# Optimization experiments

Measured on AMD Instinct MI355X. Metric: run time of the kernel, lower is better.

## Reference

```python
import jax, jax.numpy as jnp
import numpy as np

# ---- static lookup-point config (matches cfg.radius/stride/level) ----
RADIUS = [4, 4, 4, 4]
STRIDE = [1, 1, 1, 1]
LEVEL = [0, 1, 2, 3]

def _build_pts():
    pts = {}
    for r, s, l in zip(RADIUS, STRIDE, LEVEL):
        pts.setdefault(l, set())
        for x in range(-r, r + 1):
            for y in range(-r, r + 1):
                pts[l].add((x * s, y * s))
    # sorted() reproduces torch's `v.sort()` on (x, y) tuples
    return {l: np.array(sorted(v), dtype=np.float32) for l, v in sorted(pts.items())}

PTS = _build_pts()                       # {lvl: (n_lvl, 2) offsets in level pixels}
N_LEVELS = max(LEVEL) + 1                # 4
CORR_DIM = 2 * sum(len(v) for v in PTS.values())   # 648
C_HALF = CORR_DIM // 2                   # 324 = per-direction channels
B, C, H, W = 1, 256, 80, 80


def _bilinear_sample(corr, x, y):
    """corr: (B, P, h, w); x, y: (P, n) pixel coords (align_corners=False convention,
    already converted to pixel space). Zero padding outside. Returns (B, P, n)."""
    Bn, P, h, w = corr.shape
    cf = corr.reshape(Bn, P, h * w)
    x0 = jnp.floor(x)
    y0 = jnp.floor(y)
    wx1 = x - x0
    wy1 = y - y0
    x0i = x0.astype(jnp.int32)
    y0i = y0.astype(jnp.int32)
    out = jnp.zeros((Bn, P, x.shape[-1]), corr.dtype)
    for dx, wxx in ((0, 1.0 - wx1), (1, wx1)):
        for dy, wyy in ((0, 1.0 - wy1), (1, wy1)):
            xi = x0i + dx
            yi = y0i + dy
            valid = (xi >= 0) & (xi < w) & (yi >= 0) & (yi < h)
            idx = jnp.clip(yi, 0, h - 1) * w + jnp.clip(xi, 0, w - 1)   # (P, n)
            v = jnp.take_along_axis(cf, jnp.broadcast_to(idx[None], (Bn,) + idx.shape), axis=2)
            out = out + v * (wxx * wyy * valid)[None]
    return out


def _lookup_pyramid(pyr):
    """pyr[lvl]: (B, P, H>>lvl, W>>lvl). Returns (B, P, C_HALF)."""
    outs = []
    for lvl, pts in PTS.items():
        s = 1 << lvl
        n = pts.shape[0]
        dxy = jnp.asarray(pts)
        # grid_sample align_corners=False: level-pixel coord of full-res pixel j is
        # (2j+1)/(2s) - 0.5; neighbor offsets are exactly `pts` in level pixels.
        bx = (2.0 * jnp.arange(W) + 1.0) / (2.0 * s) - 0.5   # (W,)
        by = (2.0 * jnp.arange(H) + 1.0) / (2.0 * s) - 0.5   # (H,)
        x = jnp.broadcast_to(bx[None, :, None] + dxy[None, None, :, 0], (H, W, n)).reshape(H * W, n)
        y = jnp.broadcast_to(by[:, None, None] + dxy[None, None, :, 1], (H, W, n)).reshape(H * W, n)
        outs.append(_bilinear_sample(pyr[lvl], x, y))
    return jnp.concatenate(outs, axis=-1)


def _pyramid(corr):
    """corr: (B, P, H, W) -> list of avg-pooled levels (2x2, stride 2)."""
    p = [corr]
    for _ in range(N_LEVELS - 1):
        b, pp, h, w = corr.shape
        corr = corr.reshape(b, pp, h // 2, 2, w // 2, 2).mean(axis=(3, 5))
        p.append(corr)
    return p


def _conv3x3_relu(x, w, b):
    y = jax.lax.conv_general_dilated(x, w, (1, 1), 'SAME',
                                     dimension_numbers=('NHWC', 'HWIO', 'NHWC'))
    return jax.nn.relu(y + b)


def _layer_norm(x, g, b, eps=1e-5):
    m = x.mean(-1, keepdims=True)
    v = ((x - m) ** 2).mean(-1, keepdims=True)
    return (x - m) * jax.lax.rsqrt(v + eps) * g + b


def setup_inputs() -> dict:
    key = jax.random.key(0)
    ks = jax.random.split(key, 4)
    return {
        'f0': jax.random.normal(ks[0], (B, C, H, W), jnp.float32),
        'f1': jax.random.normal(ks[1], (B, C, H, W), jnp.float32),
        'conv_w1': jax.random.normal(ks[2], (3, 3, C_HALF, C_HALF), jnp.float32) * 0.02,
        'conv_b1': jnp.zeros((C_HALF,), jnp.float32),
        'conv_w2': jax.random.normal(ks[3], (3, 3, C_HALF, C_HALF), jnp.float32) * 0.02,
        'conv_b2': jnp.zeros((C_HALF,), jnp.float32),
        'ln_g': jnp.ones((C_HALF,), jnp.float32),
        'ln_b': jnp.zeros((C_HALF,), jnp.float32),
    }


def reference(f0, f1, conv_w1, conv_b1, conv_w2, conv_b2, ln_g, ln_b):
    Bn, Cn, Hn, Wn = f0.shape
    P = Hn * Wn
    a = f0.reshape(Bn, Cn, P)
    bb = f1.reshape(Bn, Cn, P)
    corr01 = jnp.einsum('bcp,bcq->bpq', a, bb)          # (B, P, P)
    corr10 = jnp.swapaxes(corr01, 1, 2)
    feat01 = _lookup_pyramid(_pyramid(corr01.reshape(Bn, P, Hn, Wn)))   # (B, P, C_HALF)
    feat10 = _lookup_pyramid(_pyramid(corr10.reshape(Bn, P, Hn, Wn)))

    def branch(feat):
        x = feat.reshape(Bn, Hn, Wn, C_HALF)
        y = x + _conv3x3_relu(_conv3x3_relu(x, conv_w1, conv_b1), conv_w2, conv_b2)
        y = _layer_norm(y, ln_g, ln_b)
        return jnp.transpose(y, (0, 3, 1, 2))           # (B, C_HALF, H, W)

    return jnp.concatenate([branch(feat01), branch(feat10)], axis=1)    # (B, 2*C_HALF, H, W)
```

## Files before the change

kernel.cpp:

```cpp
#include <hip/hip_runtime.h>

typedef unsigned short u16;
typedef unsigned int   u32;
typedef float f32x4 __attribute__((ext_vector_type(4)));
typedef __bf16 bf16x8 __attribute__((ext_vector_type(8)));
typedef unsigned short u16x8 __attribute__((ext_vector_type(8)));

#define PP   6400
#define HH   80
#define WW   80
#define KC   256
#define CH   324
#define CPAD 384
#define PW   82
#define PPIX (PW*PW)
#define NP2  896

__device__ inline float b2f(u16 u) { union { u32 i; float f; } v; v.i = ((u32)u) << 16; return v.f; }
__device__ inline u16 f2b(float f) {
    union { u32 i; float f; } v; v.f = f;
    u32 r = v.i + 0x7fffu + ((v.i >> 16) & 1u);
    return (u16)(r >> 16);
}

__device__ __forceinline__ void gload16(const void* g, void* l) {
    __builtin_amdgcn_global_load_lds((const __attribute__((address_space(1))) void*)g,
                                     (__attribute__((address_space(3))) void*)l, 16, 0, 0);
}

__global__ __launch_bounds__(256) void prep_f(const float* __restrict__ f0,
                                              const float* __restrict__ f1,
                                              u16* __restrict__ fA, u16* __restrict__ fB) {
    __shared__ float tile[64][65];
    int p0 = blockIdx.x * 64, c0 = blockIdx.y * 64;
    const float* src = blockIdx.z ? f1 : f0;
    u16* dst = blockIdx.z ? fB : fA;
    int tid = threadIdx.x;
#pragma unroll
    for (int it = 0; it < 16; ++it) {
        int idx = tid + it * 256;
        int cc = idx >> 6, pp = idx & 63;
        tile[cc][pp] = src[(size_t)(c0 + cc) * PP + p0 + pp];
    }
    __syncthreads();
#pragma unroll
    for (int it = 0; it < 16; ++it) {
        int idx = tid + it * 256;
        int pp = idx >> 6, cc = idx & 63;
        dst[(size_t)(p0 + pp) * KC + c0 + cc] = f2b(tile[cc][pp]);
    }
}

__global__ __launch_bounds__(256) void prep_w(const float* __restrict__ w1,
                                              const float* __restrict__ w2,
                                              u16* __restrict__ wT1, u16* __restrict__ wT2) {
    __shared__ float tile[64][65];
    int tap = blockIdx.x;
    int t6 = blockIdx.y;
    int ci0 = (t6 / 6) * 64, co0 = (t6 % 6) * 64;
    const float* w = blockIdx.z ? w2 : w1;
    u16* wT = blockIdx.z ? wT2 : wT1;
    int tid = threadIdx.x;
#pragma unroll
    for (int it = 0; it < 16; ++it) {
        int idx = tid + it * 256;
        int ciL = idx >> 6, coL = idx & 63;
        int ci = ci0 + ciL, co = co0 + coL;
        tile[ciL][coL] = (ci < CH && co < CH) ? w[((size_t)tap * CH + ci) * CH + co] : 0.f;
    }
    __syncthreads();
#pragma unroll
    for (int it = 0; it < 16; ++it) {
        int idx = tid + it * 256;
        int coL = idx >> 6, ciL = idx & 63;
        wT[((size_t)tap * CPAD + co0 + coL) * CPAD + ci0 + ciL] = f2b(tile[ciL][coL]);
    }
}

__global__ __launch_bounds__(384) void zero_border(u16* __restrict__ feat, u16* __restrict__ t1,
                                                   const float* __restrict__ b1,
                                                   const float* __restrict__ b2,
                                                   float* __restrict__ b1p, float* __restrict__ b2p) {
    int bi = blockIdx.x, dir = blockIdx.y;
    int t = threadIdx.x;
    if (bi == 324) {
        if (dir == 0) b1p[t] = t < CH ? b1[t] : 0.f;
        else          b2p[t] = t < CH ? b2[t] : 0.f;
        return;
    }
    int pix;
    if (bi < 82) pix = bi;
    else if (bi < 164) pix = 81 * PW + (bi - 82);
    else if (bi < 244) pix = (bi - 164 + 1) * PW;
    else pix = (bi - 244 + 1) * PW + 81;
    size_t off = ((size_t)dir * PPIX + pix) * CPAD + t;
    feat[off] = 0;
    t1[off] = 0;
}

__global__ __launch_bounds__(256) void pool_feat(const u16* __restrict__ fA,
                                                 const u16* __restrict__ fB,
                                                 u16* __restrict__ pbarA,
                                                 u16* __restrict__ pbarB) {
    int j = blockIdx.x;
    const u16* src = blockIdx.y ? fA : fB;
    u16* dst = blockIdx.y ? pbarA : pbarB;
    int k = threadIdx.x;
    int cy3 = j / 10, cx3 = j % 10;
    float l1v[16], l2v[4];
#pragma unroll
    for (int a = 0; a < 4; ++a)
#pragma unroll
        for (int b = 0; b < 4; ++b) {
            int cy = cy3 * 4 + a, cx = cx3 * 4 + b;
            int p00 = (2 * cy) * 80 + 2 * cx;
            float v = 0.25f * (b2f(src[(size_t)p00 * KC + k]) + b2f(src[(size_t)(p00 + 1) * KC + k]) +
                               b2f(src[(size_t)(p00 + 80) * KC + k]) + b2f(src[(size_t)(p00 + 81) * KC + k]));
            l1v[a * 4 + b] = v;
            dst[(size_t)(cy * 40 + cx) * KC + k] = f2b(v);
        }
#pragma unroll
    for (int a = 0; a < 2; ++a)
#pragma unroll
        for (int b = 0; b < 2; ++b) {
            float v = 0.25f * (l1v[(2 * a) * 4 + 2 * b] + l1v[(2 * a) * 4 + 2 * b + 1] +
                               l1v[(2 * a + 1) * 4 + 2 * b] + l1v[(2 * a + 1) * 4 + 2 * b + 1]);
            l2v[a * 2 + b] = v;
            dst[(size_t)(1600 + (cy3 * 2 + a) * 20 + cx3 * 2 + b) * KC + k] = f2b(v);
        }
    float v3 = 0.25f * (l2v[0] + l2v[1] + l2v[2] + l2v[3]);
    dst[(size_t)(2000 + j) * KC + k] = f2b(v3);
}

__global__ __launch_bounds__(256) void gemm_cp(const u16* __restrict__ fA,
                                               const u16* __restrict__ fB,
                                               const u16* __restrict__ pbarA,
                                               const u16* __restrict__ pbarB,
                                               u16* __restrict__ corr01,
                                               u16* __restrict__ corr10,
                                               u16* __restrict__ pc) {
    int y = blockIdx.y, z = blockIdx.z;
    bool band = (y < 7);
    int m0 = blockIdx.x * 128, n0 = 0, jbase = 0;
    const u16 *Aptr, *Bptr;
    if (band) {
        if (z) return;
        int n0t = (int)blockIdx.x + y - 3;
        if (n0t < 0 || n0t >= 50) return;
        n0 = n0t * 128;
        Aptr = fA; Bptr = fB;
    } else {
        jbase = (y - 7) * 128;
        Aptr = z ? fB : fA;
        Bptr = z ? pbarA : pbarB;
    }
    int py0 = m0 / 80;
    int s1 = min(max(py0 / 2 - 5, 0), 28);
    int s2 = min(max(py0 / 4 - 5, 0), 8);

    __shared__ __align__(16) char smem[128 * 136 * 2];
    u16* As = (u16*)smem;
    u16* Bs = As + 128 * 64;
    u16* trans = (u16*)smem;
    const int TS = 136;
    int tid = threadIdx.x;
    int wave = tid >> 6, lane = tid & 63;
    int quad = lane >> 4, l16 = lane & 15;
    int lrow = lane >> 3, lchunk = lane & 7;
    int sc = lchunk ^ (lrow & 7);
    int sw = l16 & 7;
    int wr = (wave >> 1) * 64, wc = (wave & 1) * 64;
    f32x4 acc[4][4] = {};

    size_t gRow[4];
#pragma unroll
    for (int i = 0; i < 4; ++i) {
        int row = i * 32 + wave * 8 + lrow;
        if (band) gRow[i] = (size_t)(n0 + row);
        else {
            int j = jbase + row;
            int g = j < 480 ? s1 * 40 + j
                  : j < 720 ? 1120 + s2 * 20 + j
                  : j < 820 ? 1280 + j
                  : 2099;
            gRow[i] = (size_t)g;
        }
    }

    for (int k0 = 0; k0 < KC; k0 += 64) {
        __syncthreads();
#pragma unroll
        for (int i = 0; i < 4; ++i) {
            int row = i * 32 + wave * 8 + lrow;
            gload16(&Aptr[(size_t)(m0 + row) * KC + k0 + sc * 8], &As[(i * 32 + wave * 8) * 64]);
            gload16(&Bptr[gRow[i] * KC + k0 + sc * 8], &Bs[(i * 32 + wave * 8) * 64]);
        }
        __syncthreads();
#pragma unroll
        for (int ki = 0; ki < 2; ++ki) {
            bf16x8 af[4], bfr[4];
#pragma unroll
            for (int mi = 0; mi < 4; ++mi) {
                int r = wr + mi * 16 + l16;
                af[mi] = *(const bf16x8*)(&As[r * 64 + (((ki * 4 + quad) ^ sw) * 8)]);
            }
#pragma unroll
            for (int ni = 0; ni < 4; ++ni) {
                int r = wc + ni * 16 + l16;
                bfr[ni] = *(const bf16x8*)(&Bs[r * 64 + (((ki * 4 + quad) ^ sw) * 8)]);
            }
#pragma unroll
            for (int mi = 0; mi < 4; ++mi)
#pragma unroll
                for (int ni = 0; ni < 4; ++ni)
                    acc[mi][ni] = __builtin_amdgcn_mfma_f32_16x16x32_bf16(af[mi], bfr[ni], acc[mi][ni], 0, 0, 0);
        }
    }
    __syncthreads();
#pragma unroll
    for (int mi = 0; mi < 4; ++mi)
#pragma unroll
        for (int ni = 0; ni < 4; ++ni) {
            int rbase = wr + mi * 16 + quad * 4;
            int c = wc + ni * 16 + l16;
#pragma unroll
            for (int rr = 0; rr < 4; ++rr)
                trans[(rbase + rr) * TS + c] = f2b(acc[mi][ni][rr]);
        }
    __syncthreads();
    if (!band) {
        int dir = z;
#pragma unroll
        for (int it = 0; it < 8; ++it) {
            int r = it * 16 + (tid >> 4);
            int c8 = (tid & 15) * 8;
            u16x8 v = *(const u16x8*)(&trans[r * TS + c8]);
            *(u16x8*)(&pc[((size_t)dir * PP + m0 + r) * NP2 + jbase + c8]) = v;
        }
        return;
    }
#pragma unroll
    for (int it = 0; it < 8; ++it) {
        int r = it * 16 + (tid >> 4);
        int c8 = (tid & 15) * 8;
        u16x8 v = *(const u16x8*)(&trans[r * TS + c8]);
        *(u16x8*)(&corr01[(size_t)(m0 + r) * PP + n0 + c8]) = v;
    }
    __syncthreads();
#pragma unroll
    for (int mi = 0; mi < 4; ++mi)
#pragma unroll
        for (int ni = 0; ni < 4; ++ni) {
            int c = wc + ni * 16 + l16;
            int rbase = wr + mi * 16 + quad * 4;
#pragma unroll
            for (int h = 0; h < 2; ++h) {
                u32 pk = (u32)f2b(acc[mi][ni][2 * h]) | ((u32)f2b(acc[mi][ni][2 * h + 1]) << 16);
                *(u32*)(&trans[c * TS + rbase + 2 * h]) = pk;
            }
        }
    __syncthreads();
#pragma unroll
    for (int it = 0; it < 8; ++it) {
        int c = it * 16 + (tid >> 4);
        int r8 = (tid & 15) * 8;
        u16x8 v = *(const u16x8*)(&trans[c * TS + r8]);
        *(u16x8*)(&corr10[(size_t)(n0 + c) * PP + m0 + r8]) = v;
    }
}

__global__ __launch_bounds__(384) void lookup(const u16* __restrict__ corr01,
                                              const u16* __restrict__ corr10,
                                              const u16* __restrict__ pc,
                                              u16* __restrict__ feat) {
    __shared__ __align__(16) u16 pcrow[4][NP2];
    __shared__ float l0buf[4][81];
    int p0 = blockIdx.x * 4, dir = blockIdx.y;
    int tid = threadIdx.x;
    const u16* corr = dir ? corr10 : corr01;
    int mt = p0 >> 7;
    int py0 = (mt * 128) / 80;
    int s1 = min(max(py0 / 2 - 5, 0), 28);
    int s2 = min(max(py0 / 4 - 5, 0), 8);
    for (int i = tid; i < 4 * (NP2 / 8); i += 384) {
        int j = i / (NP2 / 8), cc = i % (NP2 / 8);
        *(u16x8*)(&pcrow[j][cc * 8]) =
            *(const u16x8*)(&pc[((size_t)dir * PP + p0 + j) * NP2 + cc * 8]);
    }
    if (tid < 324) {
        int j = tid / 81, i = tid % 81;
        int p = p0 + j;
        int px = p % WW, py = p / WW;
        int dy = i / 9 - 4, dx = i % 9 - 4;
        int x = px + dx, yy = py + dy;
        float v = 0.f;
        if ((unsigned)x < (unsigned)WW && (unsigned)yy < (unsigned)HH)
            v = b2f(corr[(size_t)p * PP + yy * WW + x]);
        l0buf[j][(i % 9) * 9 + i / 9] = v;
    }
    __syncthreads();
    int ch = tid;
#pragma unroll
    for (int j = 0; j < 4; ++j) {
        int p = p0 + j;
        int px = p % WW, py = p / WW;
        float val = 0.f;
        if (ch < CH) {
            int lvl = ch / 81, i = ch % 81;
            if (lvl == 0) {
                val = l0buf[j][i];
            } else {
                int dx = i / 9 - 4, dy = i % 9 - 4;
                int wl = WW >> lvl;
                float inv = 1.0f / (float)(2 << lvl);
                float xc = (float)(2 * px + 1) * inv - 0.5f + (float)dx;
                float yc = (float)(2 * py + 1) * inv - 0.5f + (float)dy;
                float x0f = floorf(xc), y0f = floorf(yc);
                int x0 = (int)x0f, y0 = (int)y0f;
                float wx = xc - x0f, wy = yc - y0f;
#pragma unroll
                for (int cy = 0; cy < 2; ++cy)
#pragma unroll
                    for (int cx = 0; cx < 2; ++cx) {
                        int xi = x0 + cx, yi = y0 + cy;
                        if ((unsigned)xi < (unsigned)wl && (unsigned)yi < (unsigned)wl) {
                            float wgt = (cx ? wx : 1.f - wx) * (cy ? wy : 1.f - wy);
                            int idx = (lvl == 1) ? (yi - s1) * 40 + xi
                                    : (lvl == 2) ? 480 + (yi - s2) * 20 + xi
                                                 : 720 + yi * 10 + xi;
                            val += b2f(pcrow[j][idx]) * wgt;
                        }
                    }
            }
        }
        size_t pix = (size_t)(py + 1) * PW + px + 1;
        feat[((size_t)dir * PPIX + pix) * CPAD + ch] = f2b(val);
    }
}

__global__ __launch_bounds__(256) void conv_gemm(const u16* __restrict__ inFeat,
                                                 const u16* __restrict__ wTt,
                                                 const float* __restrict__ bias,
                                                 const u16* __restrict__ resid,
                                                 u16* __restrict__ outb) {
    int L = (int)blockIdx.x;
    int xcd = L & 7;
    int q = L >> 3;
    int n_t = q % 3; q /= 3;
    int mg = q % 13;
    int dir = q / 13;
    int m_t = mg * 8 + xcd;
    if (m_t >= 100) return;
    const u16* Ain = inFeat + (size_t)dir * PPIX * CPAD;
    const u16* Rin = resid ? resid + (size_t)dir * PPIX * CPAD : (const u16*)0;
    u16* Out = outb + (size_t)dir * PPIX * CPAD;
    __shared__ __align__(16) u16 As[64 * 128];
    __shared__ __align__(16) u16 Bs[128 * 128];
    int tid = threadIdx.x;
    int wave = tid >> 6, lane = tid & 63;
    int quad = lane >> 4, l16 = lane & 15;
    int wr = (wave >> 1) * 32, wc = (wave & 1) * 64;
    int m0 = m_t * 64, n0 = n_t * 128;
    f32x4 acc[2][4] = {};

    int pixA[4], scI[4];
#pragma unroll
    for (int i = 0; i < 4; ++i) {
        int r = wave * 16 + i * 4 + quad;
        int m = m0 + r;
        pixA[i] = (m / 80 + 1) * PW + (m % 80) + 1;
        scI[i] = l16 ^ ((i * 4 + quad) & 15);
    }

    for (int tap = 0; tap < 9; ++tap) {
        int dpix = (tap / 3 - 1) * PW + (tap % 3) - 1;
        const u16* Wt = wTt + ((size_t)tap * CPAD + n0) * CPAD;
#pragma unroll
        for (int kt = 0; kt < 3; ++kt) {
            int kc = kt * 128;
            __syncthreads();
#pragma unroll
            for (int i = 0; i < 4; ++i)
                gload16(&Ain[(size_t)(pixA[i] + dpix) * CPAD + kc + scI[i] * 8],
                        &As[(wave * 16 + i * 4) * 128]);
#pragma unroll
            for (int j = 0; j < 8; ++j) {
                int rb = wave * 32 + j * 4;
                gload16(&Wt[(size_t)(rb + quad) * CPAD + kc + scI[j & 3] * 8],
                        &Bs[rb * 128]);
            }
            __syncthreads();
#pragma unroll
            for (int ki = 0; ki < 4; ++ki) {
                int slot = (ki * 4 + quad) ^ l16;
                bf16x8 af[2], bfr[4];
#pragma unroll
                for (int mi = 0; mi < 2; ++mi)
                    af[mi] = *(const bf16x8*)(&As[(wr + mi * 16 + l16) * 128 + slot * 8]);
#pragma unroll
                for (int ni = 0; ni < 4; ++ni)
                    bfr[ni] = *(const bf16x8*)(&Bs[(wc + ni * 16 + l16) * 128 + slot * 8]);
#pragma unroll
                for (int mi = 0; mi < 2; ++mi)
#pragma unroll
                    for (int ni = 0; ni < 4; ++ni)
                        acc[mi][ni] = __builtin_amdgcn_mfma_f32_16x16x32_bf16(af[mi], bfr[ni], acc[mi][ni], 0, 0, 0);
            }
        }
    }
#pragma unroll
    for (int mi = 0; mi < 2; ++mi)
#pragma unroll
        for (int rr = 0; rr < 4; ++rr) {
            int p = m0 + wr + mi * 16 + quad * 4 + rr;
            size_t opix = (size_t)(p / 80 + 1) * PW + (p % 80) + 1;
#pragma unroll
            for (int ni = 0; ni < 4; ++ni) {
                int co = n0 + wc + ni * 16 + l16;
                float v = acc[mi][ni][rr] + bias[co];
                v = fmaxf(v, 0.f);
                if (Rin) v += b2f(Rin[opix * CPAD + co]);
                Out[opix * CPAD + co] = f2b(v);
            }
        }
}

__global__ __launch_bounds__(256) void ln_out(const u16* __restrict__ t2,
                                              const float* __restrict__ g,
                                              const float* __restrict__ b,
                                              float* __restrict__ out) {
    int dir = blockIdx.y;
    int p0 = blockIdx.x * 64;
    const u16* Y = t2 + (size_t)dir * PPIX * CPAD;
    __shared__ u16 buf[64 * 325];
    __shared__ float mean_s[64], inv_s[64];
    __shared__ float part[64][4][2];
    int tid = threadIdx.x;
    for (int idx = tid; idx < 64 * CH; idx += 256) {
        int pp = idx / CH, c = idx - pp * CH;
        int p = p0 + pp;
        size_t pix = (size_t)(p / 80 + 1) * PW + (p % 80) + 1;
        buf[pp * 325 + c] = Y[pix * CPAD + c];
    }
    __syncthreads();
    {
        int pp = tid >> 2, q = tid & 3;
        float s = 0.f, s2 = 0.f;
        for (int c = q; c < CH; c += 4) { float v = b2f(buf[pp * 325 + c]); s += v; s2 += v * v; }
        part[pp][q][0] = s; part[pp][q][1] = s2;
    }
    __syncthreads();
    if (tid < 64) {
        float s = 0.f, s2 = 0.f;
        for (int q = 0; q < 4; ++q) { s += part[tid][q][0]; s2 += part[tid][q][1]; }
        float m = s / (float)CH;
        float var = s2 / (float)CH - m * m;
        if (var < 0.f) var = 0.f;
        mean_s[tid] = m;
        inv_s[tid] = rsqrtf(var + 1e-5f);
    }
    __syncthreads();
    for (int idx = tid; idx < CH * 64; idx += 256) {
        int c = idx >> 6, pp = idx & 63;
        float v = (b2f(buf[pp * 325 + c]) - mean_s[pp]) * inv_s[pp] * g[c] + b[c];
        out[((size_t)(dir * CH + c)) * PP + p0 + pp] = v;
    }
}

extern "C" void kernel_launch(void* const* d_in, const int* in_sizes, int n_in,
                              void* d_out, int out_size, void* d_ws, size_t ws_size,
                              hipStream_t stream) {
    const float* f0  = (const float*)d_in[0];
    const float* f1  = (const float*)d_in[1];
    const float* w1  = (const float*)d_in[2];
    const float* b1  = (const float*)d_in[3];
    const float* w2  = (const float*)d_in[4];
    const float* b2  = (const float*)d_in[5];
    const float* lng = (const float*)d_in[6];
    const float* lnb = (const float*)d_in[7];
    float* out = (float*)d_out;

    char* ws = (char*)d_ws;
    size_t off = 0;
    auto alloc = [&](size_t bytes) -> char* {
        char* r = ws + off;
        off += (bytes + 511) & ~(size_t)511;
        return r;
    };
    u16* fA     = (u16*)alloc((size_t)PP * KC * 2);
    u16* fB     = (u16*)alloc((size_t)PP * KC * 2);
    u16* corr01 = (u16*)alloc((size_t)PP * PP * 2);
    u16* corr10 = (u16*)alloc((size_t)PP * PP * 2);
    u16* pc     = (u16*)alloc((size_t)2 * PP * NP2 * 2);
    u16* feat   = (u16*)alloc((size_t)2 * PPIX * CPAD * 2);
    u16* t1     = (u16*)alloc((size_t)2 * PPIX * CPAD * 2);
    u16* t2     = (u16*)alloc((size_t)2 * PPIX * CPAD * 2);
    u16* pbarA  = (u16*)alloc((size_t)2176 * KC * 2);
    u16* pbarB  = (u16*)alloc((size_t)2176 * KC * 2);
    u16* wT1    = (u16*)alloc((size_t)9 * CPAD * CPAD * 2);
    u16* wT2    = (u16*)alloc((size_t)9 * CPAD * CPAD * 2);
    float* b1p  = (float*)alloc(CPAD * 4);
    float* b2p  = (float*)alloc(CPAD * 4);

    prep_f<<<dim3(100, 4, 2), 256, 0, stream>>>(f0, f1, fA, fB);
    prep_w<<<dim3(9, 36, 2), 256, 0, stream>>>(w1, w2, wT1, wT2);
    zero_border<<<dim3(325, 2), 384, 0, stream>>>(feat, t1, b1, b2, b1p, b2p);
    pool_feat<<<dim3(100, 2), 256, 0, stream>>>(fA, fB, pbarA, pbarB);
    gemm_cp<<<dim3(50, 14, 2), 256, 0, stream>>>(fA, fB, pbarA, pbarB, corr01, corr10, pc);
    lookup<<<dim3(1600, 2), 384, 0, stream>>>(corr01, corr10, pc, feat);
    conv_gemm<<<dim3(624), 256, 0, stream>>>(feat, wT1, b1p, (const u16*)0, t1);
    conv_gemm<<<dim3(624), 256, 0, stream>>>(t1, wT2, b2p, feat, t2);
    ln_out<<<dim3(100, 2), 256, 0, stream>>>(t2, lng, lnb, out);
}
```

Before: 247.5 us.

## Write level-0 correlation window directly from GEMM epilogue, drop full corr buffers

The band GEMM tiles now scatter only the 9x9 neighbourhood values into both direction feature buffers, instead of writing full dense corr01/corr10 tiles. The lookup kernel no longer reads the large correlation matrices for level 0; it only zeroes out-of-range neighbours. This removes large global writes and reads and the transpose staging. In exchange it uses scattered 2-byte stores and relies on write ordering between the two kernels for the zeroed entries.

```diff
diff --git a/kernel.cpp b/kernel.cpp
--- a/kernel.cpp
+++ b/kernel.cpp
@@ -136,9 +136,8 @@
                                                const u16* __restrict__ fB,
                                                const u16* __restrict__ pbarA,
                                                const u16* __restrict__ pbarB,
-                                               u16* __restrict__ corr01,
-                                               u16* __restrict__ corr10,
-                                               u16* __restrict__ pc) {
+                                               u16* __restrict__ pc,
+                                               u16* __restrict__ feat) {
     int y = blockIdx.y, z = blockIdx.z;
     bool band = (y < 7);
     int m0 = blockIdx.x * 128, n0 = 0, jbase = 0;
@@ -216,6 +215,31 @@
                     acc[mi][ni] = __builtin_amdgcn_mfma_f32_16x16x32_bf16(af[mi], bfr[ni], acc[mi][ni], 0, 0, 0);
         }
     }
+    if (band) {
+        u16* fd0 = feat;
+        u16* fd1 = feat + (size_t)PPIX * CPAD;
+#pragma unroll
+        for (int ni = 0; ni < 4; ++ni) {
+            int q = n0 + wc + ni * 16 + l16;
+            int qy = q / 80, qx = q - qy * 80;
+            size_t qpix = (size_t)((qy + 1) * PW + qx + 1) * CPAD;
+#pragma unroll
+            for (int mi = 0; mi < 4; ++mi)
+#pragma unroll
+                for (int rr = 0; rr < 4; ++rr) {
+                    int p = m0 + wr + mi * 16 + quad * 4 + rr;
+                    int py = p / 80, px = p - py * 80;
+                    int dx = qx - px, dy = qy - py;
+                    if ((unsigned)(dx + 4) < 9u && (unsigned)(dy + 4) < 9u) {
+                        u16 v = f2b(acc[mi][ni][rr]);
+                        size_t ppix = (size_t)((py + 1) * PW + px + 1) * CPAD;
+                        fd0[ppix + (dx + 4) * 9 + (dy + 4)] = v;
+                        fd1[qpix + (4 - dx) * 9 + (4 - dy)] = v;
+                    }
+                }
+        }
+        return;
+    }
     __syncthreads();
 #pragma unroll
     for (int mi = 0; mi < 4; ++mi)
@@ -228,7 +252,7 @@
                 trans[(rbase + rr) * TS + c] = f2b(acc[mi][ni][rr]);
         }
     __syncthreads();
-    if (!band) {
+    {
         int dir = z;
 #pragma unroll
         for (int it = 0; it < 8; ++it) {
@@ -237,47 +261,14 @@
             u16x8 v = *(const u16x8*)(&trans[r * TS + c8]);
             *(u16x8*)(&pc[((size_t)dir * PP + m0 + r) * NP2 + jbase + c8]) = v;
         }
-        return;
-    }
-#pragma unroll
-    for (int it = 0; it < 8; ++it) {
-        int r = it * 16 + (tid >> 4);
-        int c8 = (tid & 15) * 8;
-        u16x8 v = *(const u16x8*)(&trans[r * TS + c8]);
-        *(u16x8*)(&corr01[(size_t)(m0 + r) * PP + n0 + c8]) = v;
-    }
-    __syncthreads();
-#pragma unroll
-    for (int mi = 0; mi < 4; ++mi)
-#pragma unroll
-        for (int ni = 0; ni < 4; ++ni) {
-            int c = wc + ni * 16 + l16;
-            int rbase = wr + mi * 16 + quad * 4;
-#pragma unroll
-            for (int h = 0; h < 2; ++h) {
-                u32 pk = (u32)f2b(acc[mi][ni][2 * h]) | ((u32)f2b(acc[mi][ni][2 * h + 1]) << 16);
-                *(u32*)(&trans[c * TS + rbase + 2 * h]) = pk;
-            }
-        }
-    __syncthreads();
-#pragma unroll
-    for (int it = 0; it < 8; ++it) {
-        int c = it * 16 + (tid >> 4);
-        int r8 = (tid & 15) * 8;
-        u16x8 v = *(const u16x8*)(&trans[c * TS + r8]);
-        *(u16x8*)(&corr10[(size_t)(n0 + c) * PP + m0 + r8]) = v;
-    }
-}
-
-__global__ __launch_bounds__(384) void lookup(const u16* __restrict__ corr01,
-                                              const u16* __restrict__ corr10,
-                                              const u16* __restrict__ pc,
+    }
+}
+
+__global__ __launch_bounds__(384) void lookup(const u16* __restrict__ pc,
                                               u16* __restrict__ feat) {
     __shared__ __align__(16) u16 pcrow[4][NP2];
-    __shared__ float l0buf[4][81];
     int p0 = blockIdx.x * 4, dir = blockIdx.y;
     int tid = threadIdx.x;
-    const u16* corr = dir ? corr10 : corr01;
     int mt = p0 >> 7;
     int py0 = (mt * 128) / 80;
     int s1 = min(max(py0 / 2 - 5, 0), 28);
@@ -287,54 +278,46 @@
         *(u16x8*)(&pcrow[j][cc * 8]) =
             *(const u16x8*)(&pc[((size_t)dir * PP + p0 + j) * NP2 + cc * 8]);
     }
-    if (tid < 324) {
-        int j = tid / 81, i = tid % 81;
-        int p = p0 + j;
-        int px = p % WW, py = p / WW;
-        int dy = i / 9 - 4, dx = i % 9 - 4;
-        int x = px + dx, yy = py + dy;
-        float v = 0.f;
-        if ((unsigned)x < (unsigned)WW && (unsigned)yy < (unsigned)HH)
-            v = b2f(corr[(size_t)p * PP + yy * WW + x]);
-        l0buf[j][(i % 9) * 9 + i / 9] = v;
-    }
     __syncthreads();
     int ch = tid;
 #pragma unroll
     for (int j = 0; j < 4; ++j) {
         int p = p0 + j;
         int px = p % WW, py = p / WW;
-        float val = 0.f;
-        if (ch < CH) {
+        size_t pix = (size_t)(py + 1) * PW + px + 1;
+        if (ch < 81) {
+            int dx = ch / 9 - 4, dy = ch % 9 - 4;
+            int x = px + dx, yy = py + dy;
+            if ((unsigned)x >= (unsigned)WW || (unsigned)yy >= (unsigned)HH)
+                feat[((size_t)dir * PPIX + pix) * CPAD + ch] = 0;
+        } else if (ch < CH) {
             int lvl = ch / 81, i = ch % 81;
-            if (lvl == 0) {
-                val = l0buf[j][i];
-            } else {
-                int dx = i / 9 - 4, dy = i % 9 - 4;
-                int wl = WW >> lvl;
-                float inv = 1.0f / (float)(2 << lvl);
-                float xc = (float)(2 * px + 1) * inv - 0.5f + (float)dx;
-                float yc = (float)(2 * py + 1) * inv - 0.5f + (float)dy;
-                float x0f = floorf(xc), y0f = floorf(yc);
-                int x0 = (int)x0f, y0 = (int)y0f;
-                float wx = xc - x0f, wy = yc - y0f;
-#pragma unroll
-                for (int cy = 0; cy < 2; ++cy)
-#pragma unroll
-                    for (int cx = 0; cx < 2; ++cx) {
-                        int xi = x0 + cx, yi = y0 + cy;
-                        if ((unsigned)xi < (unsigned)wl && (unsigned)yi < (unsigned)wl) {
-                            float wgt = (cx ? wx : 1.f - wx) * (cy ? wy : 1.f - wy);
-                            int idx = (lvl == 1) ? (yi - s1) * 40 + xi
-                                    : (lvl == 2) ? 480 + (yi - s2) * 20 + xi
-                                                 : 720 + yi * 10 + xi;
-                            val += b2f(pcrow[j][idx]) * wgt;
-                        }
+            int dx = i / 9 - 4, dy = i % 9 - 4;
+            int wl = WW >> lvl;
+            float inv = 1.0f / (float)(2 << lvl);
+            float xc = (float)(2 * px + 1) * inv - 0.5f + (float)dx;
+            float yc = (float)(2 * py + 1) * inv - 0.5f + (float)dy;
+            float x0f = floorf(xc), y0f = floorf(yc);
+            int x0 = (int)x0f, y0 = (int)y0f;
+            float wx = xc - x0f, wy = yc - y0f;
+            float val = 0.f;
+#pragma unroll
+            for (int cy = 0; cy < 2; ++cy)
+#pragma unroll
+                for (int cx = 0; cx < 2; ++cx) {
+                    int xi = x0 + cx, yi = y0 + cy;
+                    if ((unsigned)xi < (unsigned)wl && (unsigned)yi < (unsigned)wl) {
+                        float wgt = (cx ? wx : 1.f - wx) * (cy ? wy : 1.f - wy);
+                        int idx = (lvl == 1) ? (yi - s1) * 40 + xi
+                                : (lvl == 2) ? 480 + (yi - s2) * 20 + xi
+                                             : 720 + yi * 10 + xi;
+                        val += b2f(pcrow[j][idx]) * wgt;
                     }
-            }
-        }
-        size_t pix = (size_t)(py + 1) * PW + px + 1;
-        feat[((size_t)dir * PPIX + pix) * CPAD + ch] = f2b(val);
+                }
+            feat[((size_t)dir * PPIX + pix) * CPAD + ch] = f2b(val);
+        } else {
+            feat[((size_t)dir * PPIX + pix) * CPAD + ch] = 0;
+        }
     }
 }
 
@@ -489,8 +472,6 @@
     };
     u16* fA     = (u16*)alloc((size_t)PP * KC * 2);
     u16* fB     = (u16*)alloc((size_t)PP * KC * 2);
-    u16* corr01 = (u16*)alloc((size_t)PP * PP * 2);
-    u16* corr10 = (u16*)alloc((size_t)PP * PP * 2);
     u16* pc     = (u16*)alloc((size_t)2 * PP * NP2 * 2);
     u16* feat   = (u16*)alloc((size_t)2 * PPIX * CPAD * 2);
     u16* t1     = (u16*)alloc((size_t)2 * PPIX * CPAD * 2);
@@ -506,8 +487,8 @@
     prep_w<<<dim3(9, 36, 2), 256, 0, stream>>>(w1, w2, wT1, wT2);
     zero_border<<<dim3(325, 2), 384, 0, stream>>>(feat, t1, b1, b2, b1p, b2p);
     pool_feat<<<dim3(100, 2), 256, 0, stream>>>(fA, fB, pbarA, pbarB);
-    gemm_cp<<<dim3(50, 14, 2), 256, 0, stream>>>(fA, fB, pbarA, pbarB, corr01, corr10, pc);
-    lookup<<<dim3(1600, 2), 384, 0, stream>>>(corr01, corr10, pc, feat);
+    gemm_cp<<<dim3(50, 14, 2), 256, 0, stream>>>(fA, fB, pbarA, pbarB, pc, feat);
+    lookup<<<dim3(1600, 2), 384, 0, stream>>>(pc, feat);
     conv_gemm<<<dim3(624), 256, 0, stream>>>(feat, wT1, b1p, (const u16*)0, t1);
     conv_gemm<<<dim3(624), 256, 0, stream>>>(t1, wT2, b2p, feat, t2);
     ln_out<<<dim3(100, 2), 256, 0, stream>>>(t2, lng, lnb, out);
```

Result: no change. 246.0 us (-0.6%).
